# Performance work log

Measured on AMD Instinct MI355X. Metric: run time of the kernel, lower is better.

## Reference

```python
import jax, jax.numpy as jnp
import numpy as np

N_NODES = 50000
N_EDGES = 600000
D = 128
EPS = 1e-5
AVG_D_LOG = float(np.log(4 + 1))  # avg_d={'log': log(avg_d+1)}, avg_d=4


def setup_inputs() -> dict:
    key = jax.random.key(0)
    ks = jax.random.split(key, 8)
    h = jax.random.normal(ks[0], (N_NODES, D), dtype=jnp.float32)
    # guarantee every node has at least one incoming edge (self-loop)
    edge_dst = jnp.concatenate([
        jnp.arange(N_NODES, dtype=jnp.int64),
        jax.random.randint(ks[1], (N_EDGES - N_NODES,), 0, N_NODES).astype(jnp.int64),
    ])
    edge_src = jax.random.randint(ks[2], (N_EDGES,), 0, N_NODES).astype(jnp.int64)
    def lin(k, fan_in, fan_out):
        lim = 1.0 / np.sqrt(fan_in)
        return jax.random.uniform(k, (fan_in, fan_out), jnp.float32, -lim, lim)
    W_pre = lin(ks[3], 2 * D, D)
    b_pre = jnp.zeros((D,), jnp.float32)
    W_post = lin(ks[4], 12 * D + D, D)  # 4 aggregators * 3 scalers * D + in_dim
    b_post = jnp.zeros((D,), jnp.float32)
    W_mix = lin(ks[5], D, D)
    b_mix = jnp.zeros((D,), jnp.float32)
    return {"h": h, "edge_src": edge_src, "edge_dst": edge_dst,
            "W_pre": W_pre, "b_pre": b_pre, "W_post": W_post,
            "b_post": b_post, "W_mix": W_mix, "b_mix": b_mix}


def reference(h, edge_src, edge_dst, W_pre, b_pre, W_post, b_post, W_mix, b_mix):
    n = h.shape[0]
    # pretrans_edges: cat(src, dst) -> Linear -> ReLU (MLP act) -> ReLU (outer)
    z2 = jnp.concatenate([h[edge_src], h[edge_dst]], axis=1)        # [E, 2D]
    e = jax.nn.relu(z2 @ W_pre + b_pre)                             # [E, D]
    # multi-aggregator segment reduce over destination nodes
    deg = jax.ops.segment_sum(jnp.ones_like(edge_dst, jnp.float32), edge_dst, n)  # [N]
    inv_deg = 1.0 / deg[:, None]
    mean = jax.ops.segment_sum(e, edge_dst, n) * inv_deg
    mean_sq = jax.ops.segment_sum(e * e, edge_dst, n) * inv_deg
    std = jnp.sqrt(jax.nn.relu(mean_sq - mean * mean) + EPS)
    mx = jax.ops.segment_max(e, edge_dst, n)
    mn = jax.ops.segment_min(e, edge_dst, n)
    agg = jnp.concatenate([mean, mx, mn, std], axis=1)              # [N, 4D]
    # scalers: identity, amplification, attenuation
    log_d = jnp.log(deg + 1.0)[:, None]
    scaled = jnp.concatenate([agg, agg * (log_d / AVG_D_LOG), agg * (AVG_D_LOG / log_d)], axis=1)  # [N, 12D]
    # posttrans: cat(h, aggregated) -> Linear -> ReLU
    hp = jax.nn.relu(jnp.concatenate([h, scaled], axis=1) @ W_post + b_post)  # [N, D]
    # mixing network + residual (node_dim == out_dim)
    out = h + jax.nn.leaky_relu(hp @ W_mix + b_mix, negative_slope=0.01)
    return out
```

## Files before the change

### kernel.cpp

```cpp
#include <hip/hip_runtime.h>
#include <hip/hip_bf16.h>

#define N_NODES 50000
#define N_EDGES 600000
#define D 128
#define NB_SCAN 196

constexpr float AVG_D_LOG = 1.6094379124341003f;
constexpr float EPS_V = 1e-5f;

#define PQ_B     0ul
#define AGG_B    25600000ul
#define HBF_B    76800000ul
#define WPRET2_B 89600000ul
#define WPOSTT_B 89665536ul
#define WMIXT_B  90091520ul
#define DEGC_B   90124288ul
#define OFF_B    90324288ul
#define CUR_B    90524352ul
#define SRCS_B   90724352ul
#define BSUM_B   93124352ul

typedef __attribute__((ext_vector_type(8))) short bf16x8;
typedef __attribute__((ext_vector_type(4))) float f32x4;

__device__ __forceinline__ short f2b(float f) {
    unsigned u = __builtin_bit_cast(unsigned, f);
    u += 0x7fffu + ((u >> 16) & 1u);
    return (short)(u >> 16);
}
__device__ __forceinline__ unsigned pk2(float a, float b) {
    return (unsigned)(unsigned short)f2b(a) | ((unsigned)(unsigned short)f2b(b) << 16);
}
__device__ __forceinline__ float blo(unsigned u) { return __uint_as_float(u << 16); }
__device__ __forceinline__ float bhi(unsigned u) { return __uint_as_float(u & 0xffff0000u); }

__global__ __launch_bounds__(256) void prep_kernel(
    const float* __restrict__ h, const float* __restrict__ Wpre,
    const float* __restrict__ Wpost, const float* __restrict__ Wmix,
    short* __restrict__ hbf, short* __restrict__ wpreT2,
    short* __restrict__ wpostT, short* __restrict__ wmixT,
    int* __restrict__ degc, int* __restrict__ cursor)
{
    long i = (long)blockIdx.x * 256 + threadIdx.x;
    if (i < 6400000) { hbf[i] = f2b(h[i]); return; }
    i -= 6400000;
    if (i < 32768) {
        int n = i >> 7, k = i & 127;
        float v = (n < 128) ? Wpre[k * 128 + n] : Wpre[(k + 128) * 128 + (n - 128)];
        wpreT2[n * 128 + k] = f2b(v);
        return;
    }
    i -= 32768;
    if (i < 212992) { int k = i >> 7, n = i & 127; wpostT[n * 1664 + k] = f2b(Wpost[k * 128 + n]); return; }
    i -= 212992;
    if (i < 16384) { int k = i >> 7, n = i & 127; wmixT[n * 128 + k] = f2b(Wmix[k * 128 + n]); return; }
    i -= 16384;
    if (i < N_NODES) { degc[i] = 0; return; }
    i -= N_NODES;
    if (i < N_NODES) cursor[i] = 0;
}

__global__ __launch_bounds__(256) void hist_kernel(const int* __restrict__ edst, int* __restrict__ degc) {
    int e = blockIdx.x * 256 + threadIdx.x;
    if (e < N_EDGES) atomicAdd(&degc[edst[e]], 1);
}

__global__ __launch_bounds__(256) void scan1_kernel(const int* __restrict__ degc, int* __restrict__ bsum) {
    int n = blockIdx.x * 256 + threadIdx.x;
    int v = (n < N_NODES) ? degc[n] : 0;
#pragma unroll
    for (int o = 32; o > 0; o >>= 1) v += __shfl_down(v, o);
    __shared__ int w4[4];
    if ((threadIdx.x & 63) == 0) w4[threadIdx.x >> 6] = v;
    __syncthreads();
    if (threadIdx.x == 0) bsum[blockIdx.x] = w4[0] + w4[1] + w4[2] + w4[3];
}

__global__ __launch_bounds__(256) void scan2_kernel(int* __restrict__ bsum, int* __restrict__ off) {
    __shared__ int sd[256];
    int tid = threadIdx.x;
    int v = (tid < NB_SCAN) ? bsum[tid] : 0;
    sd[tid] = v;
    __syncthreads();
    for (int o = 1; o < 256; o <<= 1) {
        int t = (tid >= o) ? sd[tid - o] : 0;
        __syncthreads();
        sd[tid] += t;
        __syncthreads();
    }
    if (tid < NB_SCAN) bsum[tid] = sd[tid] - v;
    if (tid == 0) off[N_NODES] = sd[255];
}

__global__ __launch_bounds__(256) void scan3_kernel(const int* __restrict__ degc,
                                                    const int* __restrict__ bsum, int* __restrict__ off) {
    __shared__ int sd[256];
    int tid = threadIdx.x;
    int n = blockIdx.x * 256 + tid;
    int v = (n < N_NODES) ? degc[n] : 0;
    sd[tid] = v;
    __syncthreads();
    for (int o = 1; o < 256; o <<= 1) {
        int t = (tid >= o) ? sd[tid - o] : 0;
        __syncthreads();
        sd[tid] += t;
        __syncthreads();
    }
    if (n < N_NODES) off[n] = sd[tid] - v + bsum[blockIdx.x];
}

__global__ __launch_bounds__(256) void scatter_kernel(const int* __restrict__ esrc, const int* __restrict__ edst,
                                                      const int* __restrict__ off, int* __restrict__ cursor,
                                                      int* __restrict__ srcs) {
    int e = blockIdx.x * 256 + threadIdx.x;
    if (e < N_EDGES) {
        int d = edst[e];
        int p = off[d] + atomicAdd(&cursor[d], 1);
        srcs[p] = esrc[e];
    }
}

__global__ __launch_bounds__(256) void gemm_pq_kernel(
    const short* __restrict__ hbf, const short* __restrict__ wpreT2,
    const float* __restrict__ bpre, short* __restrict__ PQ)
{
    __shared__ __align__(16) short As[128][72];
    __shared__ __align__(16) short Bs[128][72];

    const int tid = threadIdx.x;
    const int cg = blockIdx.x & 1;
    const int bn = (blockIdx.x >> 1) * 128;
    const int lane = tid & 63, wv = tid >> 6;
    const int lm = lane & 15, quad = lane >> 4;

    f32x4 acc[2][8];
#pragma unroll
    for (int a = 0; a < 2; a++)
#pragma unroll
        for (int b = 0; b < 8; b++) acc[a][b] = (f32x4){0.f, 0.f, 0.f, 0.f};

#pragma unroll
    for (int kc = 0; kc < 2; kc++) {
        __syncthreads();
#pragma unroll
        for (int t = 0; t < 4; t++) {
            int q = tid + t * 256;
            int m = q >> 3, seg = q & 7;
            int n = bn + m; if (n >= N_NODES) n = N_NODES - 1;
            *(int4*)&As[m][seg * 8] = *(const int4*)(hbf + (long)n * 128 + kc * 64 + seg * 8);
        }
#pragma unroll
        for (int t = 0; t < 4; t++) {
            int q = tid + t * 256;
            int n = q >> 3, seg = q & 7;
            *(int4*)&Bs[n][seg * 8] = *(const int4*)(wpreT2 + (cg * 128 + n) * 128 + kc * 64 + seg * 8);
        }
        __syncthreads();
#pragma unroll
        for (int ks = 0; ks < 2; ks++) {
            const int ko = ks * 32 + quad * 8;
            bf16x8 a0 = *(const bf16x8*)&As[wv * 32 + lm][ko];
            bf16x8 a1 = *(const bf16x8*)&As[wv * 32 + 16 + lm][ko];
#pragma unroll
            for (int ct = 0; ct < 8; ct++) {
                bf16x8 b = *(const bf16x8*)&Bs[ct * 16 + lm][ko];
                acc[0][ct] = __builtin_amdgcn_mfma_f32_16x16x32_bf16(b, a0, acc[0][ct], 0, 0, 0);
                acc[1][ct] = __builtin_amdgcn_mfma_f32_16x16x32_bf16(b, a1, acc[1][ct], 0, 0, 0);
            }
        }
    }

#pragma unroll
    for (int rt = 0; rt < 2; rt++) {
        int row = wv * 32 + rt * 16 + lm;
        int n = bn + row;
        if (n >= N_NODES) continue;
        short* dst = PQ + (long)n * 256;
#pragma unroll
        for (int ct = 0; ct < 8; ct++) {
            int col = cg * 128 + ct * 16 + quad * 4;
            float v0 = acc[rt][ct][0], v1 = acc[rt][ct][1], v2 = acc[rt][ct][2], v3 = acc[rt][ct][3];
            if (cg) {
                float4 bv = *(const float4*)(bpre + (col - 128));
                v0 += bv.x; v1 += bv.y; v2 += bv.z; v3 += bv.w;
            }
            int2 pkd; pkd.x = (int)pk2(v0, v1); pkd.y = (int)pk2(v2, v3);
            *(int2*)(dst + col) = pkd;
        }
    }
}

__global__ __launch_bounds__(256) void edgestats_kernel(
    const short* __restrict__ PQ, const int* __restrict__ srcs,
    const int* __restrict__ off, short* __restrict__ aggbf)
{
    const int wv = threadIdx.x >> 6, lane = threadIdx.x & 63;
    const int n = blockIdx.x * 4 + wv;
    const unsigned* Pb = (const unsigned*)PQ;

    const int s0 = __builtin_amdgcn_readfirstlane(off[n]);
    const int s1 = __builtin_amdgcn_readfirstlane(off[n + 1]);

    unsigned qu = Pb[(long)n * 128 + 64 + lane];
    const float qa = blo(qu), qb = bhi(qu);

    float sA = 0.f, sB = 0.f, qA = 0.f, qB = 0.f;
    float mxA = -1e30f, mxB = -1e30f, mnA = 1e30f, mnB = 1e30f;

    int p = s0;
    for (; p + 4 <= s1; p += 4) {
        int i0 = srcs[p], i1 = srcs[p + 1], i2 = srcs[p + 2], i3 = srcs[p + 3];
        unsigned u0 = Pb[(long)i0 * 128 + lane];
        unsigned u1 = Pb[(long)i1 * 128 + lane];
        unsigned u2 = Pb[(long)i2 * 128 + lane];
        unsigned u3 = Pb[(long)i3 * 128 + lane];
#pragma unroll
        for (int j = 0; j < 4; j++) {
            unsigned u = (j == 0) ? u0 : (j == 1) ? u1 : (j == 2) ? u2 : u3;
            float a = blo(u) + qa; a = a > 0.f ? a : 0.f;
            float b = bhi(u) + qb; b = b > 0.f ? b : 0.f;
            sA += a; sB += b; qA += a * a; qB += b * b;
            mxA = fmaxf(mxA, a); mxB = fmaxf(mxB, b);
            mnA = fminf(mnA, a); mnB = fminf(mnB, b);
        }
    }
    for (; p < s1; p++) {
        unsigned u = Pb[(long)srcs[p] * 128 + lane];
        float a = blo(u) + qa; a = a > 0.f ? a : 0.f;
        float b = bhi(u) + qb; b = b > 0.f ? b : 0.f;
        sA += a; sB += b; qA += a * a; qB += b * b;
        mxA = fmaxf(mxA, a); mxB = fmaxf(mxB, b);
        mnA = fminf(mnA, a); mnB = fminf(mnB, b);
    }

    float inv = 1.0f / (float)(s1 - s0);
    float mA = sA * inv, mB = sB * inv;
    float vA = qA * inv - mA * mA; vA = vA > 0.f ? vA : 0.f;
    float vB = qB * inv - mB * mB; vB = vB > 0.f ? vB : 0.f;
    float stA = sqrtf(vA + EPS_V), stB = sqrtf(vB + EPS_V);

    unsigned* ag = (unsigned*)(aggbf + (long)n * 512);
    ag[lane]       = pk2(mA, mB);
    ag[64 + lane]  = pk2(mxA, mxB);
    ag[128 + lane] = pk2(mnA, mnB);
    ag[192 + lane] = pk2(stA, stB);
}

__global__ __launch_bounds__(256) void node_kernel(
    const float* __restrict__ h, const short* __restrict__ hbf, const short* __restrict__ aggbf,
    const int* __restrict__ degc, const short* __restrict__ wpostT, const float* __restrict__ bpost,
    const short* __restrict__ wmixT, const float* __restrict__ bmix, float* __restrict__ out)
{
    __shared__ __align__(16) short As[64][72];
    __shared__ __align__(16) short Bs[128][72];
    __shared__ float sAmp[64], sAtt[64];

    const int tid = threadIdx.x;
    const int bn = blockIdx.x * 64;
    if (tid < 64) {
        int n = bn + tid; if (n >= N_NODES) n = N_NODES - 1;
        float d = (float)degc[n];
        float ld = logf(d + 1.0f);
        sAmp[tid] = ld * (1.0f / AVG_D_LOG);
        sAtt[tid] = AVG_D_LOG / ld;
    }
    __syncthreads();

    const int lane = tid & 63, wv = tid >> 6;
    const int rg = wv & 1, cg = wv >> 1;
    const int lm = lane & 15, quad = lane >> 4;

    f32x4 acc[2][4];
#pragma unroll
    for (int a = 0; a < 2; a++)
#pragma unroll
        for (int b = 0; b < 4; b++) acc[a][b] = (f32x4){0.f, 0.f, 0.f, 0.f};

    for (int c = 0; c < 26; c++) {
        __syncthreads();
        const int r = c >> 1;
        const int half = (c & 1) * 64;
#pragma unroll
        for (int t = 0; t < 2; t++) {
            int q = tid + t * 256;
            int m = q >> 3, seg = q & 7;
            int n = bn + m; if (n >= N_NODES) n = N_NODES - 1;
            int4 v;
            if (r == 0) {
                v = *(const int4*)(hbf + (long)n * 128 + half + seg * 8);
            } else {
                int a = (r - 1) & 3, s = (r - 1) >> 2;
                v = *(const int4*)(aggbf + (long)n * 512 + a * 128 + half + seg * 8);
                if (s) {
                    float sc = (s == 1) ? sAmp[m] : sAtt[m];
                    unsigned* pu = (unsigned*)&v;
#pragma unroll
                    for (int j = 0; j < 4; j++) {
                        unsigned u = pu[j];
                        pu[j] = pk2(blo(u) * sc, bhi(u) * sc);
                    }
                }
            }
            *(int4*)&As[m][seg * 8] = v;
        }
#pragma unroll
        for (int t = 0; t < 4; t++) {
            int q = tid + t * 256;
            int n = q >> 3, seg = q & 7;
            *(int4*)&Bs[n][seg * 8] = *(const int4*)(wpostT + n * 1664 + c * 64 + seg * 8);
        }
        __syncthreads();
#pragma unroll
        for (int ks = 0; ks < 2; ks++) {
            const int ko = ks * 32 + quad * 8;
            bf16x8 a0 = *(const bf16x8*)&As[rg * 32 + lm][ko];
            bf16x8 a1 = *(const bf16x8*)&As[rg * 32 + 16 + lm][ko];
#pragma unroll
            for (int ct = 0; ct < 4; ct++) {
                bf16x8 b = *(const bf16x8*)&Bs[cg * 64 + ct * 16 + lm][ko];
                acc[0][ct] = __builtin_amdgcn_mfma_f32_16x16x32_bf16(b, a0, acc[0][ct], 0, 0, 0);
                acc[1][ct] = __builtin_amdgcn_mfma_f32_16x16x32_bf16(b, a1, acc[1][ct], 0, 0, 0);
            }
        }
    }

#pragma unroll
    for (int rt = 0; rt < 2; rt++)
#pragma unroll
        for (int ct = 0; ct < 4; ct++) {
            float4 bv = *(const float4*)(bpost + cg * 64 + ct * 16 + quad * 4);
            float v0 = acc[rt][ct][0] + bv.x; acc[rt][ct][0] = v0 > 0.f ? v0 : 0.f;
            float v1 = acc[rt][ct][1] + bv.y; acc[rt][ct][1] = v1 > 0.f ? v1 : 0.f;
            float v2 = acc[rt][ct][2] + bv.z; acc[rt][ct][2] = v2 > 0.f ? v2 : 0.f;
            float v3 = acc[rt][ct][3] + bv.w; acc[rt][ct][3] = v3 > 0.f ? v3 : 0.f;
        }

    f32x4 acc2[2][4];
#pragma unroll
    for (int a = 0; a < 2; a++)
#pragma unroll
        for (int b = 0; b < 4; b++) acc2[a][b] = (f32x4){0.f, 0.f, 0.f, 0.f};

#pragma unroll
    for (int kc = 0; kc < 2; kc++) {
        __syncthreads();
        if (cg == kc) {
#pragma unroll
            for (int ct = 0; ct < 4; ct++) {
#pragma unroll
                for (int rt = 0; rt < 2; rt++) {
                    int row = rg * 32 + rt * 16 + lm;
                    int col = ct * 16 + quad * 4;
                    int2 pkd;
                    pkd.x = (int)pk2(acc[rt][ct][0], acc[rt][ct][1]);
                    pkd.y = (int)pk2(acc[rt][ct][2], acc[rt][ct][3]);
                    *(int2*)&As[row][col] = pkd;
                }
            }
        }
#pragma unroll
        for (int t = 0; t < 4; t++) {
            int q = tid + t * 256;
            int n = q >> 3, seg = q & 7;
            *(int4*)&Bs[n][seg * 8] = *(const int4*)(wmixT + n * 128 + kc * 64 + seg * 8);
        }
        __syncthreads();
#pragma unroll
        for (int ks = 0; ks < 2; ks++) {
            const int ko = ks * 32 + quad * 8;
            bf16x8 a0 = *(const bf16x8*)&As[rg * 32 + lm][ko];
            bf16x8 a1 = *(const bf16x8*)&As[rg * 32 + 16 + lm][ko];
#pragma unroll
            for (int ct = 0; ct < 4; ct++) {
                bf16x8 b = *(const bf16x8*)&Bs[cg * 64 + ct * 16 + lm][ko];
                acc2[0][ct] = __builtin_amdgcn_mfma_f32_16x16x32_bf16(b, a0, acc2[0][ct], 0, 0, 0);
                acc2[1][ct] = __builtin_amdgcn_mfma_f32_16x16x32_bf16(b, a1, acc2[1][ct], 0, 0, 0);
            }
        }
    }

#pragma unroll
    for (int rt = 0; rt < 2; rt++) {
        int row = rg * 32 + rt * 16 + lm;
        int n = bn + row;
        if (n >= N_NODES) continue;
#pragma unroll
        for (int ct = 0; ct < 4; ct++) {
            int col = cg * 64 + ct * 16 + quad * 4;
            float4 bv = *(const float4*)(bmix + col);
            float4 hv = *(const float4*)(h + (long)n * 128 + col);
            float4 o;
            float v0 = acc2[rt][ct][0] + bv.x; v0 = v0 > 0.f ? v0 : 0.01f * v0; o.x = hv.x + v0;
            float v1 = acc2[rt][ct][1] + bv.y; v1 = v1 > 0.f ? v1 : 0.01f * v1; o.y = hv.y + v1;
            float v2 = acc2[rt][ct][2] + bv.z; v2 = v2 > 0.f ? v2 : 0.01f * v2; o.z = hv.z + v2;
            float v3 = acc2[rt][ct][3] + bv.w; v3 = v3 > 0.f ? v3 : 0.01f * v3; o.w = hv.w + v3;
            *(float4*)(out + (long)n * 128 + col) = o;
        }
    }
}

extern "C" void kernel_launch(void* const* d_in, const int* in_sizes, int n_in,
                              void* d_out, int out_size, void* d_ws, size_t ws_size,
                              hipStream_t stream) {
    const float* h     = (const float*)d_in[0];
    const int*   esrc  = (const int*)d_in[1];
    const int*   edst  = (const int*)d_in[2];
    const float* Wpre  = (const float*)d_in[3];
    const float* bpre  = (const float*)d_in[4];
    const float* Wpost = (const float*)d_in[5];
    const float* bpost = (const float*)d_in[6];
    const float* Wmix  = (const float*)d_in[7];
    const float* bmix  = (const float*)d_in[8];
    float* out = (float*)d_out;
    char* ws = (char*)d_ws;

    short* PQ     = (short*)(ws + PQ_B);
    short* aggbf  = (short*)(ws + AGG_B);
    short* hbf    = (short*)(ws + HBF_B);
    short* wpreT2 = (short*)(ws + WPRET2_B);
    short* wpostT = (short*)(ws + WPOSTT_B);
    short* wmixT  = (short*)(ws + WMIXT_B);
    int*   degc   = (int*)(ws + DEGC_B);
    int*   off    = (int*)(ws + OFF_B);
    int*   cursor = (int*)(ws + CUR_B);
    int*   srcs   = (int*)(ws + SRCS_B);
    int*   bsum   = (int*)(ws + BSUM_B);

    prep_kernel<<<26415, 256, 0, stream>>>(h, Wpre, Wpost, Wmix, hbf, wpreT2, wpostT, wmixT, degc, cursor);
    hist_kernel<<<(N_EDGES + 255) / 256, 256, 0, stream>>>(edst, degc);
    scan1_kernel<<<NB_SCAN, 256, 0, stream>>>(degc, bsum);
    scan2_kernel<<<1, 256, 0, stream>>>(bsum, off);
    scan3_kernel<<<NB_SCAN, 256, 0, stream>>>(degc, bsum, off);
    scatter_kernel<<<(N_EDGES + 255) / 256, 256, 0, stream>>>(esrc, edst, off, cursor, srcs);
    gemm_pq_kernel<<<((N_NODES + 127) / 128) * 2, 256, 0, stream>>>(hbf, wpreT2, bpre, PQ);
    edgestats_kernel<<<N_NODES / 4, 256, 0, stream>>>(PQ, srcs, off, aggbf);
    node_kernel<<<(N_NODES + 63) / 64, 256, 0, stream>>>(h, hbf, aggbf, degc, wpostT, bpost, wmixT, bmix, out);
}
```

Before: 297.5 us.

## Restructure node GEMM: factor degree scalers out, async LDS loads, 128-row tiles

The node kernel no longer rescales the aggregate tile for the amplification and attenuation blocks. Each aggregate tile is loaded once and multiplied against three weight slices into separate identity, amplification and attenuation accumulators, which are combined with per-row scalers in the epilogue. Tiles are staged with direct global-to-LDS loads into XOR-swizzled, double-buffered LDS, and each block now covers 128 rows with each wave owning full columns. This cuts repeated A-tile loads and bf16 rescale work, but triples accumulator register use, which risks spills and lower occupancy.

```diff
diff --git a/kernel.cpp b/kernel.cpp
--- a/kernel.cpp
+++ b/kernel.cpp
@@ -34,6 +34,12 @@
 }
 __device__ __forceinline__ float blo(unsigned u) { return __uint_as_float(u << 16); }
 __device__ __forceinline__ float bhi(unsigned u) { return __uint_as_float(u & 0xffff0000u); }
+
+__device__ __forceinline__ void gld_lds16(const void* g, void* l) {
+    __builtin_amdgcn_global_load_lds(
+        (const __attribute__((address_space(1))) void*)g,
+        (__attribute__((address_space(3))) void*)l, 16, 0, 0);
+}
 
 __global__ __launch_bounds__(256) void prep_kernel(
     const float* __restrict__ h, const float* __restrict__ Wpre,
@@ -247,154 +253,167 @@
     ag[192 + lane] = pk2(stA, stB);
 }
 
-__global__ __launch_bounds__(256) void node_kernel(
+
+__device__ __forceinline__ void stageA_t(short* ldsT, const short* src, int rs, int co,
+                                         int bn, int wv, int lane) {
+    const int sub = lane >> 3, seg = lane & 7;
+    const int sg = (seg ^ sub) * 8;
+#pragma unroll
+    for (int t = 0; t < 4; t++) {
+        int i = wv * 4 + t;
+        int row = i * 8 + sub;
+        int n = bn + row; if (n >= N_NODES) n = N_NODES - 1;
+        gld_lds16(src + (long)n * rs + co + sg, ldsT + i * 512);
+    }
+}
+__device__ __forceinline__ void stageB_t(short* ldsT, const short* src, int rs, int co,
+                                         int wv, int lane) {
+    const int sub = lane >> 3, seg = lane & 7;
+    const int sg = (seg ^ sub) * 8;
+#pragma unroll
+    for (int t = 0; t < 4; t++) {
+        int i = wv * 4 + t;
+        int row = i * 8 + sub;
+        gld_lds16(src + (long)row * rs + co + sg, ldsT + i * 512);
+    }
+}
+
+#define MFMA_ITER(AB, BB, ACC)                                                      \
+    {                                                                               \
+        _Pragma("unroll")                                                           \
+        for (int ks = 0; ks < 2; ks++) {                                            \
+            const int qx = (((ks * 4 + quad) ^ r7) * 8);                            \
+            bf16x8 a0 = *(const bf16x8*)&(AB)[(wv * 32 + lm) * 64 + qx];            \
+            bf16x8 a1 = *(const bf16x8*)&(AB)[(wv * 32 + 16 + lm) * 64 + qx];       \
+            _Pragma("unroll")                                                       \
+            for (int ct = 0; ct < 8; ct++) {                                        \
+                bf16x8 b = *(const bf16x8*)&(BB)[(ct * 16 + lm) * 64 + qx];         \
+                ACC[0][ct] = __builtin_amdgcn_mfma_f32_16x16x32_bf16(b, a0, ACC[0][ct], 0, 0, 0); \
+                ACC[1][ct] = __builtin_amdgcn_mfma_f32_16x16x32_bf16(b, a1, ACC[1][ct], 0, 0, 0); \
+            }                                                                       \
+        }                                                                           \
+    }
+
+__global__ __launch_bounds__(256, 2) void node_kernel(
     const float* __restrict__ h, const short* __restrict__ hbf, const short* __restrict__ aggbf,
     const int* __restrict__ degc, const short* __restrict__ wpostT, const float* __restrict__ bpost,
     const short* __restrict__ wmixT, const float* __restrict__ bmix, float* __restrict__ out)
 {
-    __shared__ __align__(16) short As[64][72];
-    __shared__ __align__(16) short Bs[128][72];
-    __shared__ float sAmp[64], sAtt[64];
+    __shared__ __align__(16) short As[2][8192];
+    __shared__ __align__(16) short Bs[2][8192];
+    __shared__ float sAmp[128], sAtt[128];
 
     const int tid = threadIdx.x;
-    const int bn = blockIdx.x * 64;
-    if (tid < 64) {
+    const int bn = blockIdx.x * 128;
+    const int lane = tid & 63, wv = tid >> 6;
+    const int lm = lane & 15, quad = lane >> 4;
+    const int r7 = lm & 7;
+
+    if (tid < 128) {
         int n = bn + tid; if (n >= N_NODES) n = N_NODES - 1;
         float d = (float)degc[n];
         float ld = logf(d + 1.0f);
         sAmp[tid] = ld * (1.0f / AVG_D_LOG);
         sAtt[tid] = AVG_D_LOG / ld;
     }
-    __syncthreads();
-
-    const int lane = tid & 63, wv = tid >> 6;
-    const int rg = wv & 1, cg = wv >> 1;
-    const int lm = lane & 15, quad = lane >> 4;
-
-    f32x4 acc[2][4];
+
+    f32x4 accI[2][8], accM[2][8], accT[2][8];
 #pragma unroll
     for (int a = 0; a < 2; a++)
 #pragma unroll
-        for (int b = 0; b < 4; b++) acc[a][b] = (f32x4){0.f, 0.f, 0.f, 0.f};
-
-    for (int c = 0; c < 26; c++) {
-        __syncthreads();
-        const int r = c >> 1;
-        const int half = (c & 1) * 64;
-#pragma unroll
-        for (int t = 0; t < 2; t++) {
-            int q = tid + t * 256;
-            int m = q >> 3, seg = q & 7;
-            int n = bn + m; if (n >= N_NODES) n = N_NODES - 1;
-            int4 v;
-            if (r == 0) {
-                v = *(const int4*)(hbf + (long)n * 128 + half + seg * 8);
-            } else {
-                int a = (r - 1) & 3, s = (r - 1) >> 2;
-                v = *(const int4*)(aggbf + (long)n * 512 + a * 128 + half + seg * 8);
-                if (s) {
-                    float sc = (s == 1) ? sAmp[m] : sAtt[m];
-                    unsigned* pu = (unsigned*)&v;
-#pragma unroll
-                    for (int j = 0; j < 4; j++) {
-                        unsigned u = pu[j];
-                        pu[j] = pk2(blo(u) * sc, bhi(u) * sc);
-                    }
-                }
-            }
-            *(int4*)&As[m][seg * 8] = v;
-        }
-#pragma unroll
-        for (int t = 0; t < 4; t++) {
-            int q = tid + t * 256;
-            int n = q >> 3, seg = q & 7;
-            *(int4*)&Bs[n][seg * 8] = *(const int4*)(wpostT + n * 1664 + c * 64 + seg * 8);
-        }
-        __syncthreads();
-#pragma unroll
-        for (int ks = 0; ks < 2; ks++) {
-            const int ko = ks * 32 + quad * 8;
-            bf16x8 a0 = *(const bf16x8*)&As[rg * 32 + lm][ko];
-            bf16x8 a1 = *(const bf16x8*)&As[rg * 32 + 16 + lm][ko];
-#pragma unroll
-            for (int ct = 0; ct < 4; ct++) {
-                bf16x8 b = *(const bf16x8*)&Bs[cg * 64 + ct * 16 + lm][ko];
-                acc[0][ct] = __builtin_amdgcn_mfma_f32_16x16x32_bf16(b, a0, acc[0][ct], 0, 0, 0);
-                acc[1][ct] = __builtin_amdgcn_mfma_f32_16x16x32_bf16(b, a1, acc[1][ct], 0, 0, 0);
-            }
-        }
-    }
-
-#pragma unroll
-    for (int rt = 0; rt < 2; rt++)
-#pragma unroll
-        for (int ct = 0; ct < 4; ct++) {
-            float4 bv = *(const float4*)(bpost + cg * 64 + ct * 16 + quad * 4);
-            float v0 = acc[rt][ct][0] + bv.x; acc[rt][ct][0] = v0 > 0.f ? v0 : 0.f;
-            float v1 = acc[rt][ct][1] + bv.y; acc[rt][ct][1] = v1 > 0.f ? v1 : 0.f;
-            float v2 = acc[rt][ct][2] + bv.z; acc[rt][ct][2] = v2 > 0.f ? v2 : 0.f;
-            float v3 = acc[rt][ct][3] + bv.w; acc[rt][ct][3] = v3 > 0.f ? v3 : 0.f;
-        }
-
-    f32x4 acc2[2][4];
+        for (int b = 0; b < 8; b++) {
+            accI[a][b] = (f32x4){0.f, 0.f, 0.f, 0.f};
+            accM[a][b] = (f32x4){0.f, 0.f, 0.f, 0.f};
+            accT[a][b] = (f32x4){0.f, 0.f, 0.f, 0.f};
+        }
+
+
+    stageA_t(As[0], hbf, 128, 0, bn, wv, lane);
+    stageB_t(Bs[0], wpostT, 1664, 0, wv, lane);
+    __syncthreads();
+
+    stageA_t(As[1], hbf, 128, 64, bn, wv, lane);
+    stageB_t(Bs[1], wpostT, 1664, 64, wv, lane);
+    MFMA_ITER(As[0], Bs[0], accI);
+    __syncthreads();
+
+    stageA_t(As[0], aggbf, 512, 0, bn, wv, lane);
+    stageB_t(Bs[0], wpostT, 1664, 2 * 64, wv, lane);
+    MFMA_ITER(As[1], Bs[1], accI);
+    __syncthreads();
+
+    int pb = 0;
+    for (int j = 0; j < 8; j++) {
+        short* Ac = As[j & 1];
+        if (j < 7) {
+            int jn = j + 1;
+            stageA_t(As[jn & 1], aggbf, 512, (jn >> 1) * 128 + (jn & 1) * 64, bn, wv, lane);
+        }
+        stageB_t(Bs[pb ^ 1], wpostT, 1664, (10 + j) * 64, wv, lane);
+        MFMA_ITER(Ac, Bs[pb], accI);
+        __syncthreads();
+
+        stageB_t(Bs[pb], wpostT, 1664, (18 + j) * 64, wv, lane);
+        MFMA_ITER(Ac, Bs[pb ^ 1], accM);
+        __syncthreads();
+
+        if (j < 7) stageB_t(Bs[pb ^ 1], wpostT, 1664, (3 + j) * 64, wv, lane);
+        MFMA_ITER(Ac, Bs[pb], accT);
+        __syncthreads();
+        pb ^= 1;
+    }
+
+    stageB_t(Bs[0], wmixT, 128, 0, wv, lane);
+    stageB_t(Bs[1], wmixT, 128, 64, wv, lane);
+
+    const float am0 = sAmp[wv * 32 + lm],      at0 = sAtt[wv * 32 + lm];
+    const float am1 = sAmp[wv * 32 + 16 + lm], at1 = sAtt[wv * 32 + 16 + lm];
+#pragma unroll
+    for (int rt = 0; rt < 2; rt++) {
+        const float am = rt ? am1 : am0, at = rt ? at1 : at0;
+        const int row = wv * 32 + rt * 16 + lm;
+#pragma unroll
+        for (int ct = 0; ct < 8; ct++) {
+            float4 bv = *(const float4*)(bpost + ct * 16 + quad * 4);
+            float v0 = accI[rt][ct][0] + am * accM[rt][ct][0] + at * accT[rt][ct][0] + bv.x;
+            float v1 = accI[rt][ct][1] + am * accM[rt][ct][1] + at * accT[rt][ct][1] + bv.y;
+            float v2 = accI[rt][ct][2] + am * accM[rt][ct][2] + at * accT[rt][ct][2] + bv.z;
+            float v3 = accI[rt][ct][3] + am * accM[rt][ct][3] + at * accT[rt][ct][3] + bv.w;
+            v0 = v0 > 0.f ? v0 : 0.f; v1 = v1 > 0.f ? v1 : 0.f;
+            v2 = v2 > 0.f ? v2 : 0.f; v3 = v3 > 0.f ? v3 : 0.f;
+            int2 pkd; pkd.x = (int)pk2(v0, v1); pkd.y = (int)pk2(v2, v3);
+            const int cb = (ct & 3) * 32 + quad * 8;
+            const int sb = ((((cb >> 4) ^ r7) << 4) | (cb & 15));
+            *(int2*)((char*)As[ct >> 2] + row * 128 + sb) = pkd;
+        }
+    }
+    __syncthreads();
+
+    f32x4 accO[2][8];
 #pragma unroll
     for (int a = 0; a < 2; a++)
 #pragma unroll
-        for (int b = 0; b < 4; b++) acc2[a][b] = (f32x4){0.f, 0.f, 0.f, 0.f};
-
+        for (int b = 0; b < 8; b++) accO[a][b] = (f32x4){0.f, 0.f, 0.f, 0.f};
 #pragma unroll
     for (int kc = 0; kc < 2; kc++) {
-        __syncthreads();
-        if (cg == kc) {
-#pragma unroll
-            for (int ct = 0; ct < 4; ct++) {
-#pragma unroll
-                for (int rt = 0; rt < 2; rt++) {
-                    int row = rg * 32 + rt * 16 + lm;
-                    int col = ct * 16 + quad * 4;
-                    int2 pkd;
-                    pkd.x = (int)pk2(acc[rt][ct][0], acc[rt][ct][1]);
-                    pkd.y = (int)pk2(acc[rt][ct][2], acc[rt][ct][3]);
-                    *(int2*)&As[row][col] = pkd;
-                }
-            }
-        }
-#pragma unroll
-        for (int t = 0; t < 4; t++) {
-            int q = tid + t * 256;
-            int n = q >> 3, seg = q & 7;
-            *(int4*)&Bs[n][seg * 8] = *(const int4*)(wmixT + n * 128 + kc * 64 + seg * 8);
-        }
-        __syncthreads();
-#pragma unroll
-        for (int ks = 0; ks < 2; ks++) {
-            const int ko = ks * 32 + quad * 8;
-            bf16x8 a0 = *(const bf16x8*)&As[rg * 32 + lm][ko];
-            bf16x8 a1 = *(const bf16x8*)&As[rg * 32 + 16 + lm][ko];
-#pragma unroll
-            for (int ct = 0; ct < 4; ct++) {
-                bf16x8 b = *(const bf16x8*)&Bs[cg * 64 + ct * 16 + lm][ko];
-                acc2[0][ct] = __builtin_amdgcn_mfma_f32_16x16x32_bf16(b, a0, acc2[0][ct], 0, 0, 0);
-                acc2[1][ct] = __builtin_amdgcn_mfma_f32_16x16x32_bf16(b, a1, acc2[1][ct], 0, 0, 0);
-            }
-        }
+        MFMA_ITER(As[kc], Bs[kc], accO);
     }
 
 #pragma unroll
     for (int rt = 0; rt < 2; rt++) {
-        int row = rg * 32 + rt * 16 + lm;
+        int row = wv * 32 + rt * 16 + lm;
         int n = bn + row;
         if (n >= N_NODES) continue;
 #pragma unroll
-        for (int ct = 0; ct < 4; ct++) {
-            int col = cg * 64 + ct * 16 + quad * 4;
+        for (int ct = 0; ct < 8; ct++) {
+            int col = ct * 16 + quad * 4;
             float4 bv = *(const float4*)(bmix + col);
             float4 hv = *(const float4*)(h + (long)n * 128 + col);
             float4 o;
-            float v0 = acc2[rt][ct][0] + bv.x; v0 = v0 > 0.f ? v0 : 0.01f * v0; o.x = hv.x + v0;
-            float v1 = acc2[rt][ct][1] + bv.y; v1 = v1 > 0.f ? v1 : 0.01f * v1; o.y = hv.y + v1;
-            float v2 = acc2[rt][ct][2] + bv.z; v2 = v2 > 0.f ? v2 : 0.01f * v2; o.z = hv.z + v2;
-            float v3 = acc2[rt][ct][3] + bv.w; v3 = v3 > 0.f ? v3 : 0.01f * v3; o.w = hv.w + v3;
+            float v0 = accO[rt][ct][0] + bv.x; v0 = v0 > 0.f ? v0 : 0.01f * v0; o.x = hv.x + v0;
+            float v1 = accO[rt][ct][1] + bv.y; v1 = v1 > 0.f ? v1 : 0.01f * v1; o.y = hv.y + v1;
+            float v2 = accO[rt][ct][2] + bv.z; v2 = v2 > 0.f ? v2 : 0.01f * v2; o.z = hv.z + v2;
+            float v3 = accO[rt][ct][3] + bv.w; v3 = v3 > 0.f ? v3 : 0.01f * v3; o.w = hv.w + v3;
             *(float4*)(out + (long)n * 128 + col) = o;
         }
     }
@@ -435,5 +454,5 @@
     scatter_kernel<<<(N_EDGES + 255) / 256, 256, 0, stream>>>(esrc, edst, off, cursor, srcs);
     gemm_pq_kernel<<<((N_NODES + 127) / 128) * 2, 256, 0, stream>>>(hbf, wpreT2, bpre, PQ);
     edgestats_kernel<<<N_NODES / 4, 256, 0, stream>>>(PQ, srcs, off, aggbf);
-    node_kernel<<<(N_NODES + 63) / 64, 256, 0, stream>>>(h, hbf, aggbf, degc, wpostT, bpost, wmixT, bmix, out);
-}
+    node_kernel<<<(N_NODES + 127) / 128, 256, 0, stream>>>(h, hbf, aggbf, degc, wpostT, bpost, wmixT, bmix, out);
+}
```

Measured after the change: 266.6 us. 10.4% less time.
